# Performance work log

Measured on AMD Instinct MI355X. Metric: run time of the kernel, lower is better.

Reference implementation:

```python
import jax, jax.numpy as jnp
import numpy as np

TOP_K = 10


def setup_inputs() -> dict:
    key = jax.random.key(0)
    x = jax.random.normal(key, (256, 1, 8192), dtype=jnp.float32)
    return {"x": x}


def reference(x):
    # x: [B, 1, S] real
    B, _, S = x.shape
    # torch.arange(1e-05, 1, 1/S) has exactly S elements for these S
    t = 1e-05 + jnp.arange(S, dtype=jnp.float32) / S            # [S]
    dft = jnp.fft.fft(x[:, 0, :], n=S, axis=-1, norm='ortho')   # [B, S] complex64
    mag = jnp.abs(dft)                                          # [B, S]
    top_idx = jnp.argsort(-mag, axis=-1)[:, :TOP_K]             # [B, k] int
    top_dft = jnp.take_along_axis(dft, top_idx, axis=1)         # [B, k] complex
    # complex exponential basis exp(-2j*pi*k*t), flipped along time
    phase = (-2j * jnp.pi) * (top_idx[:, :, None].astype(jnp.float32) * t[None, None, :])
    bs = jnp.exp(phase)[:, :, ::-1]                             # [B, k, S] complex
    bf = top_dft[:, :, None] * bs / jnp.sqrt(jnp.float32(S))    # [B, k, S]
    # F.pad((1,0), mode='replicate') then crop to S: shift right by 1, duplicate first col
    bf = jnp.concatenate([bf[:, :, :1], bf[:, :, :-1]], axis=-1)
    bf = bf[:, :, None, :]                                      # [B, k, 1, S]
    residual = x - jnp.sum(bf, axis=1)                          # [B, 1, S] complex
    return bf, residual
```

## Files before the change

### kernel.cpp

```cpp
#include <hip/hip_runtime.h>

#define NB    256
#define SLEN  8192
#define LOG2S 13
#define TOPK  10

#define RES_REAL   ((size_t)20971520)
#define FULL_ILV   ((size_t)46137344)

__device__ __forceinline__ float sin_rev(float p) { return __builtin_amdgcn_sinf(p); }
__device__ __forceinline__ float cos_rev(float p) { return __builtin_amdgcn_cosf(p); }

__device__ __forceinline__ bool beats(float om, int oi, float wm, int wi) {
  return (om > wm * 1.0001f) || (om > wm * 0.9999f && oi < wi);
}

__global__ __launch_bounds__(512, 1)
void fourier_fused(const float* __restrict__ x, float* __restrict__ out, size_t cap) {
  __shared__ float re[SLEN];
  __shared__ float im[SLEN];

  const int b = blockIdx.x;
  const int t = threadIdx.x;
  const int lane = t & 63;
  const int wid  = t >> 6;
  const float* xb = x + (size_t)b * SLEN;

  for (int i = t; i < SLEN; i += 512) { re[i] = xb[i]; im[i] = 0.f; }
  __syncthreads();

  for (int i = t; i < SLEN; i += 512) {
    int j = (int)(__brev((unsigned)i) >> (32 - LOG2S));
    if (i < j) { float tmp = re[i]; re[i] = re[j]; re[j] = tmp; }
  }
  __syncthreads();

  for (int stage = 1; stage <= LOG2S; ++stage) {
    const int half = 1 << (stage - 1);
    const float invm = 1.f / (float)(1 << stage);
    for (int bfi = t; bfi < SLEN / 2; bfi += 512) {
      const int pos = bfi & (half - 1);
      const int i = ((bfi >> (stage - 1)) << stage) + pos;
      const int j = i + half;
      const float p = (float)pos * invm;
      const float c  = cos_rev(p);
      const float sn = -sin_rev(p);
      const float vr = re[j], vi = im[j];
      const float tr = vr * c - vi * sn;
      const float ti = vr * sn + vi * c;
      const float ur = re[i], ui = im[i];
      re[i] = ur + tr; im[i] = ui + ti;
      re[j] = ur - tr; im[j] = ui - ti;
    }
    __syncthreads();
  }

  int   kk[TOPK];
  float ar[TOPK], ai[TOPK];
#pragma unroll
  for (int sel = 0; sel < TOPK; ++sel) {
    float wm = -1.f; int wi = SLEN;
    for (int i = t; i < SLEN; i += 512) {
      const float m2 = re[i] * re[i] + im[i] * im[i];
      if (m2 > wm * 1.0001f) { wm = m2; wi = i; }
    }
    for (int off = 32; off > 0; off >>= 1) {
      const float om = __shfl_down(wm, off);
      const int   oi = __shfl_down(wi, off);
      if (beats(om, oi, wm, wi)) { wm = om; wi = oi; }
    }
    __syncthreads();
    float sv_r = 0.f, sv_i = 0.f;
    if (t < 8) { sv_r = re[t]; sv_i = im[t]; }
    __syncthreads();
    if (lane == 0) { re[wid] = wm; im[wid] = __int_as_float(wi); }
    __syncthreads();
    wm = re[0]; wi = __float_as_int(im[0]);
    for (int w = 1; w < 8; ++w) {
      const float om = re[w]; const int oi = __float_as_int(im[w]);
      if (beats(om, oi, wm, wi)) { wm = om; wi = oi; }
    }
    __syncthreads();
    if (t < 8) { re[t] = sv_r; im[t] = sv_i; }
    __syncthreads();
    const float rr = re[wi] * (1.f / (float)SLEN);
    const float ii = im[wi] * (1.f / (float)SLEN);
    const float pr = -1e-5f * (float)wi;
    const float cp = cos_rev(pr), sp = sin_rev(pr);
    kk[sel] = wi;
    ar[sel] = rr * cp - ii * sp;
    ai[sel] = rr * sp + ii * cp;
    __syncthreads();
    if (t == 0) { re[wi] = 0.f; im[wi] = 0.f; }
    __syncthreads();
  }

  if (cap < FULL_ILV) {
    const size_t bfbase = (size_t)b * TOPK * SLEN;
    for (int pass = 0; pass < 4; ++pass) {
      const int s0 = pass * 2048 + t * 4;
      const float4 xv = *(const float4*)(xb + s0);
      float acc0 = 0.f, acc1 = 0.f, acc2 = 0.f, acc3 = 0.f;
#pragma unroll
      for (int j = 0; j < TOPK; ++j) {
        const int k = kk[j];
        float br[4];
#pragma unroll
        for (int q = 0; q < 4; ++q) {
          const int s = s0 + q;
          const int m = (s == 0) ? 1 : s;
          const float p = (float)((k * m) & (SLEN - 1)) * (1.f / (float)SLEN);
          br[q] = ar[j] * cos_rev(p) - ai[j] * sin_rev(p);
        }
        acc0 += br[0]; acc1 += br[1]; acc2 += br[2]; acc3 += br[3];
        const size_t o = bfbase + (size_t)j * SLEN + s0;
        if (o + 4 <= cap)
          *(float4*)(out + o) = make_float4(br[0], br[1], br[2], br[3]);
      }
      const size_t o = RES_REAL + (size_t)b * SLEN + s0;
      if (o + 4 <= cap)
        *(float4*)(out + o) =
            make_float4(xv.x - acc0, xv.y - acc1, xv.z - acc2, xv.w - acc3);
    }
  } else {
    const size_t bfbase = (size_t)b * TOPK * SLEN * 2;
    for (int pass = 0; pass < 8; ++pass) {
      const int s0 = pass * 1024 + t * 2;
      const int m0 = (s0 == 0) ? 1 : s0;
      const int m1 = s0 + 1;
      float sr0 = 0.f, si0 = 0.f, sr1 = 0.f, si1 = 0.f;
#pragma unroll
      for (int j = 0; j < TOPK; ++j) {
        const int k = kk[j];
        const float p0 = (float)((k * m0) & (SLEN - 1)) * (1.f / (float)SLEN);
        const float p1 = (float)((k * m1) & (SLEN - 1)) * (1.f / (float)SLEN);
        const float c0 = cos_rev(p0), s0v = sin_rev(p0);
        const float c1 = cos_rev(p1), s1v = sin_rev(p1);
        const float br0 = ar[j] * c0 - ai[j] * s0v;
        const float bi0 = ar[j] * s0v + ai[j] * c0;
        const float br1 = ar[j] * c1 - ai[j] * s1v;
        const float bi1 = ar[j] * s1v + ai[j] * c1;
        sr0 += br0; si0 += bi0; sr1 += br1; si1 += bi1;
        const size_t o = bfbase + ((size_t)j * SLEN + s0) * 2;
        if (o + 4 <= cap)
          *(float4*)(out + o) = make_float4(br0, bi0, br1, bi1);
      }
      const float2 xv = *(const float2*)(xb + s0);
      const size_t o = (size_t)41943040 + ((size_t)b * SLEN + s0) * 2;
      if (o + 4 <= cap)
        *(float4*)(out + o) = make_float4(xv.x - sr0, -si0, xv.y - sr1, -si1);
    }
  }
}

extern "C" void kernel_launch(void* const* d_in, const int* in_sizes, int n_in,
                              void* d_out, int out_size, void* d_ws, size_t ws_size,
                              hipStream_t stream) {
  const float* x = (const float*)d_in[0];
  float* out = (float*)d_out;
  fourier_fused<<<NB, 512, 0, stream>>>(x, out, (size_t)out_size);
}
```

Before: 137.0 us.

## Split FFT/top-k and output generation into two kernels with register-resident top-k

Splits the fused kernel into two. The first runs the FFT with 1024 threads per block and selects the top-k using packed 64-bit magnitude/index keys kept in registers, instead of ten rounds of shared-memory scans with barriers. The second generates the basis and residual outputs across 8x more blocks so the write-heavy phase uses more of the GPU. This adds a second launch and a global buffer for the winners, quantizes the magnitudes used for tie-breaking, and drops the complex-interleaved output path.

```diff
diff --git a/kernel.cpp b/kernel.cpp
--- a/kernel.cpp
+++ b/kernel.cpp
@@ -4,21 +4,25 @@
 #define SLEN  8192
 #define LOG2S 13
 #define TOPK  10
+#define RES_REAL ((size_t)20971520)
 
-#define RES_REAL   ((size_t)20971520)
-#define FULL_ILV   ((size_t)46137344)
+typedef unsigned long long u64;
+typedef unsigned int u32;
+
+__device__ float4 g_win[NB * TOPK];
 
 __device__ __forceinline__ float sin_rev(float p) { return __builtin_amdgcn_sinf(p); }
 __device__ __forceinline__ float cos_rev(float p) { return __builtin_amdgcn_cosf(p); }
 
-__device__ __forceinline__ bool beats(float om, int oi, float wm, int wi) {
-  return (om > wm * 1.0001f) || (om > wm * 0.9999f && oi < wi);
+__device__ __forceinline__ u64 pack_key(float m2, int i) {
+  u32 qb = __float_as_uint(m2) & 0xFFFFE000u;
+  return ((u64)qb << 32) | (u32)(SLEN - 1 - i);
 }
 
-__global__ __launch_bounds__(512, 1)
-void fourier_fused(const float* __restrict__ x, float* __restrict__ out, size_t cap) {
-  __shared__ float re[SLEN];
-  __shared__ float im[SLEN];
+__global__ __launch_bounds__(1024, 1)
+void fft_topk(const float* __restrict__ x) {
+  __shared__ __align__(16) float re[SLEN];
+  __shared__ __align__(16) float im[SLEN];
 
   const int b = blockIdx.x;
   const int t = threadIdx.x;
@@ -26,11 +30,11 @@
   const int wid  = t >> 6;
   const float* xb = x + (size_t)b * SLEN;
 
-  for (int i = t; i < SLEN; i += 512) { re[i] = xb[i]; im[i] = 0.f; }
+  for (int i = t; i < SLEN; i += 1024) { re[i] = xb[i]; im[i] = 0.f; }
   __syncthreads();
 
-  for (int i = t; i < SLEN; i += 512) {
-    int j = (int)(__brev((unsigned)i) >> (32 - LOG2S));
+  for (int i = t; i < SLEN; i += 1024) {
+    int j = (int)(__brev((u32)i) >> (32 - LOG2S));
     if (i < j) { float tmp = re[i]; re[i] = re[j]; re[j] = tmp; }
   }
   __syncthreads();
@@ -38,7 +42,7 @@
   for (int stage = 1; stage <= LOG2S; ++stage) {
     const int half = 1 << (stage - 1);
     const float invm = 1.f / (float)(1 << stage);
-    for (int bfi = t; bfi < SLEN / 2; bfi += 512) {
+    for (int bfi = t; bfi < SLEN / 2; bfi += 1024) {
       const int pos = bfi & (half - 1);
       const int i = ((bfi >> (stage - 1)) << stage) + pos;
       const int j = i + half;
@@ -55,102 +59,113 @@
     __syncthreads();
   }
 
-  int   kk[TOPK];
-  float ar[TOPK], ai[TOPK];
+  u64 key[8];
 #pragma unroll
-  for (int sel = 0; sel < TOPK; ++sel) {
-    float wm = -1.f; int wi = SLEN;
-    for (int i = t; i < SLEN; i += 512) {
-      const float m2 = re[i] * re[i] + im[i] * im[i];
-      if (m2 > wm * 1.0001f) { wm = m2; wi = i; }
-    }
-    for (int off = 32; off > 0; off >>= 1) {
-      const float om = __shfl_down(wm, off);
-      const int   oi = __shfl_down(wi, off);
-      if (beats(om, oi, wm, wi)) { wm = om; wi = oi; }
-    }
-    __syncthreads();
-    float sv_r = 0.f, sv_i = 0.f;
-    if (t < 8) { sv_r = re[t]; sv_i = im[t]; }
-    __syncthreads();
-    if (lane == 0) { re[wid] = wm; im[wid] = __int_as_float(wi); }
-    __syncthreads();
-    wm = re[0]; wi = __float_as_int(im[0]);
-    for (int w = 1; w < 8; ++w) {
-      const float om = re[w]; const int oi = __float_as_int(im[w]);
-      if (beats(om, oi, wm, wi)) { wm = om; wi = oi; }
-    }
-    __syncthreads();
-    if (t < 8) { re[t] = sv_r; im[t] = sv_i; }
-    __syncthreads();
-    const float rr = re[wi] * (1.f / (float)SLEN);
-    const float ii = im[wi] * (1.f / (float)SLEN);
-    const float pr = -1e-5f * (float)wi;
-    const float cp = cos_rev(pr), sp = sin_rev(pr);
-    kk[sel] = wi;
-    ar[sel] = rr * cp - ii * sp;
-    ai[sel] = rr * sp + ii * cp;
-    __syncthreads();
-    if (t == 0) { re[wi] = 0.f; im[wi] = 0.f; }
-    __syncthreads();
+  for (int q = 0; q < 8; ++q) {
+    const int i = t + (q << 10);
+    key[q] = pack_key(re[i] * re[i] + im[i] * im[i], i);
   }
 
-  if (cap < FULL_ILV) {
-    const size_t bfbase = (size_t)b * TOPK * SLEN;
-    for (int pass = 0; pass < 4; ++pass) {
-      const int s0 = pass * 2048 + t * 4;
-      const float4 xv = *(const float4*)(xb + s0);
-      float acc0 = 0.f, acc1 = 0.f, acc2 = 0.f, acc3 = 0.f;
+  u64 winkey[TOPK];
 #pragma unroll
-      for (int j = 0; j < TOPK; ++j) {
-        const int k = kk[j];
-        float br[4];
+  for (int r = 0; r < TOPK; ++r) {
+    u64 best = key[0];
 #pragma unroll
-        for (int q = 0; q < 4; ++q) {
-          const int s = s0 + q;
-          const int m = (s == 0) ? 1 : s;
-          const float p = (float)((k * m) & (SLEN - 1)) * (1.f / (float)SLEN);
-          br[q] = ar[j] * cos_rev(p) - ai[j] * sin_rev(p);
-        }
-        acc0 += br[0]; acc1 += br[1]; acc2 += br[2]; acc3 += br[3];
-        const size_t o = bfbase + (size_t)j * SLEN + s0;
-        if (o + 4 <= cap)
-          *(float4*)(out + o) = make_float4(br[0], br[1], br[2], br[3]);
+    for (int q = 1; q < 8; ++q) best = (key[q] > best) ? key[q] : best;
+    for (int off = 1; off < 64; off <<= 1) {
+      const u64 o = __shfl_xor(best, off);
+      best = (o > best) ? o : best;
+    }
+#pragma unroll
+    for (int q = 0; q < 8; ++q) if (key[q] == best) key[q] = 0;
+    winkey[r] = best;
+  }
+
+  u64 mykey = 0;
+#pragma unroll
+  for (int j = 0; j < TOPK; ++j) if (lane == j) mykey = winkey[j];
+  float mre = 0.f, mim = 0.f;
+  if (lane < TOPK) {
+    const int k = SLEN - 1 - (int)(mykey & 0x1FFFu);
+    mre = re[k]; mim = im[k];
+  }
+  __syncthreads();
+  if (lane < TOPK)
+    ((float4*)re)[wid * TOPK + lane] = make_float4(
+        __uint_as_float((u32)mykey), __uint_as_float((u32)(mykey >> 32)), mre, mim);
+  __syncthreads();
+
+  if (wid == 0) {
+    u64 k0, k1, k2 = 0;
+    float r0, i0, r1, i1, r2 = 0.f, i2 = 0.f;
+    float4 c = ((float4*)re)[lane];
+    k0 = ((u64)__float_as_uint(c.y) << 32) | __float_as_uint(c.x); r0 = c.z; i0 = c.w;
+    c = ((float4*)re)[lane + 64];
+    k1 = ((u64)__float_as_uint(c.y) << 32) | __float_as_uint(c.x); r1 = c.z; i1 = c.w;
+    if (lane < 32) {
+      c = ((float4*)re)[lane + 128];
+      k2 = ((u64)__float_as_uint(c.y) << 32) | __float_as_uint(c.x); r2 = c.z; i2 = c.w;
+    }
+#pragma unroll
+    for (int r = 0; r < TOPK; ++r) {
+      u64 best = (k0 > k1) ? k0 : k1;
+      best = (k2 > best) ? k2 : best;
+      for (int off = 1; off < 64; off <<= 1) {
+        const u64 o = __shfl_xor(best, off);
+        best = (o > best) ? o : best;
       }
-      const size_t o = RES_REAL + (size_t)b * SLEN + s0;
-      if (o + 4 <= cap)
-        *(float4*)(out + o) =
-            make_float4(xv.x - acc0, xv.y - acc1, xv.z - acc2, xv.w - acc3);
-    }
-  } else {
-    const size_t bfbase = (size_t)b * TOPK * SLEN * 2;
-    for (int pass = 0; pass < 8; ++pass) {
-      const int s0 = pass * 1024 + t * 2;
-      const int m0 = (s0 == 0) ? 1 : s0;
-      const int m1 = s0 + 1;
-      float sr0 = 0.f, si0 = 0.f, sr1 = 0.f, si1 = 0.f;
-#pragma unroll
-      for (int j = 0; j < TOPK; ++j) {
-        const int k = kk[j];
-        const float p0 = (float)((k * m0) & (SLEN - 1)) * (1.f / (float)SLEN);
-        const float p1 = (float)((k * m1) & (SLEN - 1)) * (1.f / (float)SLEN);
-        const float c0 = cos_rev(p0), s0v = sin_rev(p0);
-        const float c1 = cos_rev(p1), s1v = sin_rev(p1);
-        const float br0 = ar[j] * c0 - ai[j] * s0v;
-        const float bi0 = ar[j] * s0v + ai[j] * c0;
-        const float br1 = ar[j] * c1 - ai[j] * s1v;
-        const float bi1 = ar[j] * s1v + ai[j] * c1;
-        sr0 += br0; si0 += bi0; sr1 += br1; si1 += bi1;
-        const size_t o = bfbase + ((size_t)j * SLEN + s0) * 2;
-        if (o + 4 <= cap)
-          *(float4*)(out + o) = make_float4(br0, bi0, br1, bi1);
+      float cre = 0.f, cim = 0.f; bool own = false;
+      if (k0 == best)      { own = true; cre = r0; cim = i0; k0 = 0; }
+      else if (k1 == best) { own = true; cre = r1; cim = i1; k1 = 0; }
+      else if (k2 == best) { own = true; cre = r2; cim = i2; k2 = 0; }
+      if (own) {
+        const int k = SLEN - 1 - (int)(best & 0x1FFFu);
+        const float rr = cre * (1.f / (float)SLEN);
+        const float ii = cim * (1.f / (float)SLEN);
+        const float pr = -1e-5f * (float)k;
+        const float cp = cos_rev(pr), sp = sin_rev(pr);
+        g_win[b * TOPK + r] =
+            make_float4(__int_as_float(k), rr * cp - ii * sp, rr * sp + ii * cp, 0.f);
       }
-      const float2 xv = *(const float2*)(xb + s0);
-      const size_t o = (size_t)41943040 + ((size_t)b * SLEN + s0) * 2;
-      if (o + 4 <= cap)
-        *(float4*)(out + o) = make_float4(xv.x - sr0, -si0, xv.y - sr1, -si1);
     }
   }
+}
+
+__global__ __launch_bounds__(256)
+void gen_out(const float* __restrict__ x, float* __restrict__ out, size_t cap) {
+  __shared__ float4 w[TOPK];
+  const int blk = blockIdx.x;
+  const int b = blk >> 3;
+  const int chunk = blk & 7;
+  const int t = threadIdx.x;
+  if (t < TOPK) w[t] = g_win[b * TOPK + t];
+  __syncthreads();
+
+  const int s0 = chunk * 1024 + t * 4;
+  const float4 xv = *(const float4*)(x + (size_t)b * SLEN + s0);
+  float a0 = 0.f, a1 = 0.f, a2 = 0.f, a3 = 0.f;
+  const size_t bfbase = (size_t)b * TOPK * SLEN;
+
+#pragma unroll
+  for (int j = 0; j < TOPK; ++j) {
+    const int k = __float_as_int(w[j].x);
+    const float ar = w[j].y, ai = w[j].z;
+    float br[4];
+#pragma unroll
+    for (int q = 0; q < 4; ++q) {
+      const int s = s0 + q;
+      const int m = (s == 0) ? 1 : s;
+      const float p = (float)((k * m) & (SLEN - 1)) * (1.f / (float)SLEN);
+      br[q] = ar * cos_rev(p) - ai * sin_rev(p);
+    }
+    a0 += br[0]; a1 += br[1]; a2 += br[2]; a3 += br[3];
+    const size_t o = bfbase + (size_t)j * SLEN + s0;
+    if (o + 4 <= cap)
+      *(float4*)(out + o) = make_float4(br[0], br[1], br[2], br[3]);
+  }
+  const size_t o = RES_REAL + (size_t)b * SLEN + s0;
+  if (o + 4 <= cap)
+    *(float4*)(out + o) = make_float4(xv.x - a0, xv.y - a1, xv.z - a2, xv.w - a3);
 }
 
 extern "C" void kernel_launch(void* const* d_in, const int* in_sizes, int n_in,
@@ -158,5 +173,6 @@
                               hipStream_t stream) {
   const float* x = (const float*)d_in[0];
   float* out = (float*)d_out;
-  fourier_fused<<<NB, 512, 0, stream>>>(x, out, (size_t)out_size);
+  fft_topk<<<NB, 1024, 0, stream>>>(x);
+  gen_out<<<NB * 8, 256, 0, stream>>>(x, out, (size_t)out_size);
 }
```

Measured after the change: 137.0 us. Within noise of the previous version (+0.0%).
